# Kernel tuning notes

Measured on AMD Instinct MI355X. Metric: run time of the kernel, lower is better.

## Reference

```python
import jax, jax.numpy as jnp
import numpy as np

H = 128  # per-direction hidden size; bidirectional output = 256


def sru_layer(x, W, b):
    """One bidirectional SRU layer (use_selu=1).
    x: (L, B, n_in); W: (n_in, 2H*k); b: (4H,) = [f-bias(2H), r-bias(2H)].
    """
    L, B, n_in = x.shape
    k = W.shape[1] // (2 * H)  # 4 if n_in != 2H else 3
    U = (x @ W).reshape(L, B, 2, H, k)  # (L,B,dir,H,k)
    bf = b[: 2 * H].reshape(2, H)
    br = b[2 * H :].reshape(2, H)
    # highway input: learned projection (k==4) or the input itself split per direction
    xp = U[..., 3] if k == 4 else x.reshape(L, B, 2, H)
    # time-reverse the backward direction so a single scan serves both
    Us = jnp.stack([U[:, :, 0, :, :3], U[::-1, :, 1, :, :3]], axis=2)  # (L,B,2,H,3)
    xps = jnp.stack([xp[:, :, 0], xp[::-1, :, 1]], axis=2)  # (L,B,2,H)

    def step(c, t):
        u, xpt = t
        xt = u[..., 0]
        f = jax.nn.sigmoid(u[..., 1] + bf)
        r = jax.nn.sigmoid(u[..., 2] + br)
        c = f * c + (1.0 - f) * xt
        h = r * jax.nn.selu(c) + (1.0 - r) * xpt
        return c, h

    c0 = jnp.zeros((B, 2, H), x.dtype)
    _, hs = jax.lax.scan(step, c0, (Us, xps))  # hs: (L,B,2,H)
    # un-reverse backward direction, concat directions -> (L,B,2H)
    return jnp.concatenate([hs[:, :, 0], hs[::-1, :, 1]], axis=-1)


def setup_inputs() -> dict:
    key = jax.random.key(0)
    ks = jax.random.split(key, 6)
    L, B, D = 1024, 64, 128
    inp = {
        "input": jax.random.normal(ks[0], (L, B, D), jnp.float32),
        "W0": jax.random.normal(ks[1], (D, 4 * 2 * H), jnp.float32) / np.sqrt(D),
        "b0": jnp.zeros((4 * H,), jnp.float32),
        "gamma": jnp.ones((2 * H,), jnp.float32),
        "beta": jnp.zeros((2 * H,), jnp.float32),
    }
    for i, kk in zip((1, 2, 3), ks[2:5]):
        inp[f"W{i}"] = jax.random.normal(kk, (2 * H, 3 * 2 * H), jnp.float32) / np.sqrt(2 * H)
        inp[f"b{i}"] = jnp.zeros((4 * H,), jnp.float32)
    return inp


def reference(input, W0, b0, W1, b1, W2, b2, W3, b3, gamma, beta):
    x = sru_layer(input, W0, b0)
    x = sru_layer(x, W1, b1)
    x = sru_layer(x, W2, b2)
    x = sru_layer(x, W3, b3)  # (L,B,256)
    # permute(1,2,0) + avg_pool1d over full length + squeeze == mean over time
    feats = jnp.mean(x, axis=0)  # (B,256)
    mu = jnp.mean(feats, axis=-1, keepdims=True)
    var = jnp.mean(jnp.square(feats - mu), axis=-1, keepdims=True)
    return (feats - mu) / jnp.sqrt(var + 1e-5) * gamma + beta
```

## Files before the change

### kernel.cpp

```cpp
#include <hip/hip_runtime.h>
#include <math.h>

#define HID 128
#define LSEQ 1024
#define NB 64
#define SUB 32
#define NQG (LSEQ / SUB)
#define NCH 16384

typedef __attribute__((ext_vector_type(4))) float f32x4;
typedef __attribute__((ext_vector_type(8))) short bf16x8;
typedef __attribute__((ext_vector_type(8))) unsigned short u16x8;
typedef __attribute__((ext_vector_type(4))) unsigned short u16x4;

template <int N>
__device__ __forceinline__ void vmcntN() {
    asm volatile("s_waitcnt vmcnt(%0)" :: "n"(N) : "memory");
}

__device__ __forceinline__ unsigned short f2bf(float x) {
    union { float f; unsigned int u; } a; a.f = x;
    unsigned int r = a.u + 0x7FFFu + ((a.u >> 16) & 1u);
    return (unsigned short)(r >> 16);
}
__device__ __forceinline__ float bf2f(unsigned short h) {
    union { float f; unsigned int u; } a; a.u = ((unsigned int)h) << 16;
    return a.f;
}
__device__ __forceinline__ float sigmoidf_(float x) { return 1.0f / (1.0f + __expf(-x)); }
__device__ __forceinline__ float seluf_(float x) {
    const float sc = 1.0507009873554805f, al = 1.6732632423543772f;
    return x > 0.0f ? sc * x : sc * al * (__expf(x) - 1.0f);
}

__device__ __forceinline__ void gload16(const unsigned short* g, unsigned short* l) {
    __builtin_amdgcn_global_load_lds(
        (const __attribute__((address_space(1))) unsigned int*)g,
        (__attribute__((address_space(3))) unsigned int*)l, 16, 0, 0);
}

__global__ __launch_bounds__(256) void conv_wt(const float* __restrict__ W,
                                               unsigned short* __restrict__ Wt,
                                               int K, int N, int kw) {
    int idx = blockIdx.x * 256 + threadIdx.x;
    if (idx >= K * N) return;
    int k = idx / N, n = idx - k * N;
    const int dir = n / (128 * kw);
    const int rem = n - dir * 128 * kw;
    const int h = rem / kw, j = rem - h * kw;
    const int np = dir * 128 * kw + j * 128 + h;
    Wt[(size_t)np * K + k] = f2bf(W[idx]);
}

__global__ __launch_bounds__(256) void conv_in(const float* __restrict__ in,
                                               unsigned short* __restrict__ outp,
                                               int n4) {
    int idx = blockIdx.x * 256 + threadIdx.x;
    if (idx >= n4) return;
    const float4 v = *reinterpret_cast<const float4*>(in + (size_t)idx * 4);
    u16x4 w;
    w[0] = f2bf(v.x); w[1] = f2bf(v.y); w[2] = f2bf(v.z); w[3] = f2bf(v.w);
    *(u16x4*)(outp + (size_t)idx * 4) = w;
}

template <int K, int NC>
__global__ __launch_bounds__(256) void gemm_v5(const unsigned short* __restrict__ A,
                                               const unsigned short* __restrict__ Bt,
                                               unsigned short* __restrict__ C) {
    constexpr int NN = NC / 128;
    constexpr int NT = K / 64;
    constexpr int NSTEP = 4 * NT;
    __shared__ __align__(16) unsigned short smB[NT * 128 * 64];
    __shared__ __align__(16) unsigned short smA[4][4][2048];

    const int bid = blockIdx.x;
    const int mi = bid & 7;
    const int tt = bid >> 3;
    const int n = tt % NN;
    const int mg = (tt / NN) * 8 + mi;
    const int mb = mg * 512;
    const int n0 = n * 128;

    const int tid = threadIdx.x;
    const int w = tid >> 6, l = tid & 63;
    const int rlo = l & 15, g = l >> 4;
    const int kx = (l & 7) ^ (l >> 3);
    const int kswz = (rlo & 7) * 8;

#pragma unroll
    for (int kt = 0; kt < NT; ++kt)
#pragma unroll
        for (int rd = 0; rd < 4; ++rd) {
            const int col = rd * 32 + (tid >> 3);
            const int kxb = (tid & 7) ^ ((tid >> 3) & 7);
            gload16(Bt + (size_t)(n0 + col) * K + kt * 64 + kxb * 8,
                    &smB[kt * 8192 + rd * 2048 + tid * 8]);
        }

    auto stageA = [&](int s2) {
        const int mt2 = s2 / NT, kt2 = s2 % NT, sl = s2 & 3;
        const int rowb = mb + mt2 * 128 + w * 32;
#pragma unroll
        for (int i = 0; i < 4; ++i)
            gload16(A + (size_t)(rowb + i * 8 + (l >> 3)) * K + kt2 * 64 + kx * 8,
                    &smA[w][sl][i * 512 + l * 8]);
    };

    stageA(0); stageA(1); stageA(2);
    vmcntN<8>();
    __builtin_amdgcn_sched_barrier(0);
    __builtin_amdgcn_s_barrier();
    __builtin_amdgcn_sched_barrier(0);

    f32x4 acc[2][8];
#pragma unroll
    for (int s = 0; s < NSTEP; ++s) {
        const int mt = s / NT, kt = s % NT, slot = s & 3;
        if (kt == 0) {
#pragma unroll
            for (int mf = 0; mf < 2; ++mf)
#pragma unroll
                for (int nf = 0; nf < 8; ++nf) acc[mf][nf] = (f32x4){0.f, 0.f, 0.f, 0.f};
        }
        if (s + 3 < NSTEP) { stageA(s + 3); vmcntN<12>(); }
        else if (s + 3 == NSTEP) vmcntN<8>();
        else if (s + 2 == NSTEP) vmcntN<4>();
        else                     vmcntN<0>();
        __builtin_amdgcn_sched_barrier(0);

#pragma unroll
        for (int kk = 0; kk < 2; ++kk) {
            const int koff = (kk * 32 + g * 8) ^ kswz;
            bf16x8 af[2], bff[8];
#pragma unroll
            for (int mf = 0; mf < 2; ++mf)
                af[mf] = *(const bf16x8*)(&smA[w][slot][(mf * 16 + rlo) * 64 + koff]);
#pragma unroll
            for (int nf = 0; nf < 8; ++nf)
                bff[nf] = *(const bf16x8*)(&smB[kt * 8192 + (nf * 16 + rlo) * 64 + koff]);
#pragma unroll
            for (int mf = 0; mf < 2; ++mf)
#pragma unroll
                for (int nf = 0; nf < 8; ++nf)
                    acc[mf][nf] = __builtin_amdgcn_mfma_f32_16x16x32_bf16(
                        bff[nf], af[mf], acc[mf][nf], 0, 0, 0);
        }

        if (kt == NT - 1) {
            const int rowb = mb + mt * 128 + w * 32;
#pragma unroll
            for (int mf = 0; mf < 2; ++mf) {
                const size_t rbase = (size_t)(rowb + mf * 16 + rlo) * NC + n0 + g * 4;
#pragma unroll
                for (int nf = 0; nf < 8; ++nf) {
                    u16x4 v;
                    v[0] = f2bf(acc[mf][nf][0]); v[1] = f2bf(acc[mf][nf][1]);
                    v[2] = f2bf(acc[mf][nf][2]); v[3] = f2bf(acc[mf][nf][3]);
                    *(u16x4*)(&C[rbase + nf * 16]) = v;
                }
            }
        }
    }
}

template <int NC>
__global__ __launch_bounds__(256) void scanA(const unsigned short* __restrict__ U,
                                             const float* __restrict__ bias,
                                             float* __restrict__ aArr,
                                             float* __restrict__ bArr,
                                             int dirbase, int dbstride,
                                             int chmask, int chshift, int T) {
    const int gid = blockIdx.x * 256 + threadIdx.x;
    const int fc = gid & chmask;
    const int q = gid >> chshift;
    const int dir = dirbase + (fc >> 13);
    const int b = (fc >> 7) & 63, h = fc & 127;
    const int dbase = (fc >> 13) * dbstride;
    const float bfb = bias[dir * HID + h];

    float aa = 1.0f, cc = 0.0f;
#pragma unroll 4
    for (int i = 0; i < SUB; ++i) {
        const int s = q * SUB + i;
        const int t = dir ? (T - 1 - s) : s;
        const size_t m = (size_t)t * NB + b;
        const float u0 = bf2f(U[m * NC + dbase + h]);
        const float u1 = bf2f(U[m * NC + dbase + 128 + h]);
        const float f = sigmoidf_(u1 + bfb);
        cc = f * cc + (1.0f - f) * u0;
        aa *= f;
    }
    const int fcg = dir * 8192 + (fc & 8191);
    aArr[(size_t)q * NCH + fcg] = aa;
    bArr[(size_t)q * NCH + fcg] = cc;
}

template <int Q>
__global__ __launch_bounds__(256) void scanB(const float* __restrict__ aArr,
                                             const float* __restrict__ bArr,
                                             float* __restrict__ cin,
                                             float* __restrict__ carry,
                                             int init, int fcg0) {
    const int fcg = fcg0 + blockIdx.x * 256 + threadIdx.x;
    float a[Q], bb[Q];
#pragma unroll
    for (int q = 0; q < Q; ++q) {
        a[q]  = aArr[(size_t)q * NCH + fcg];
        bb[q] = bArr[(size_t)q * NCH + fcg];
    }
    float c = init ? 0.0f : carry[fcg];
#pragma unroll
    for (int q = 0; q < Q; ++q) {
        cin[(size_t)q * NCH + fcg] = c;
        c = a[q] * c + bb[q];
    }
    carry[fcg] = c;
}

template <int NC, bool XP_FROM_U, bool ACC>
__global__ __launch_bounds__(256) void scanC(const unsigned short* __restrict__ U,
                                             const unsigned short* __restrict__ Xprev,
                                             const float* __restrict__ bias,
                                             const float* __restrict__ cin,
                                             unsigned short* __restrict__ Xout,
                                             float* __restrict__ part,
                                             int dirbase, int dbstride,
                                             int chmask, int chshift,
                                             int T, int t0, int qg0) {
    const int gid = blockIdx.x * 256 + threadIdx.x;
    const int fc = gid & chmask;
    const int q = gid >> chshift;
    const int dir = dirbase + (fc >> 13);
    const int b = (fc >> 7) & 63, h = fc & 127;
    const int dbase = (fc >> 13) * dbstride;
    const float bfb = bias[dir * HID + h];
    const float brb = bias[2 * HID + dir * HID + h];
    const int fcg = dir * 8192 + (fc & 8191);

    float c = cin[(size_t)q * NCH + fcg];
    float psum = 0.0f;
#pragma unroll 4
    for (int i = 0; i < SUB; ++i) {
        const int s = q * SUB + i;
        const int t = dir ? (T - 1 - s) : s;
        const size_t m = (size_t)t * NB + b;
        const size_t xrow = ((size_t)(t0 + t) * NB + b) * (2 * HID) + dir * HID + h;
        const float u0 = bf2f(U[m * NC + dbase + h]);
        const float u1 = bf2f(U[m * NC + dbase + 128 + h]);
        const float u2 = bf2f(U[m * NC + dbase + 256 + h]);
        float xp;
        if constexpr (XP_FROM_U) xp = bf2f(U[m * NC + dbase + 384 + h]);
        else                     xp = bf2f(Xprev[xrow]);
        const float f = sigmoidf_(u1 + bfb);
        const float r = sigmoidf_(u2 + brb);
        c = f * c + (1.0f - f) * u0;
        const float ho = r * seluf_(c) + (1.0f - r) * xp;
        if constexpr (ACC) psum += ho;
        else               Xout[xrow] = f2bf(ho);
    }
    if constexpr (ACC)
        part[(size_t)(qg0 + q) * (NB * 256) + b * 256 + dir * HID + h] = psum;
}

__global__ __launch_bounds__(256) void pool2(const float* __restrict__ part,
                                             const float* __restrict__ gamma,
                                             const float* __restrict__ beta,
                                             float* __restrict__ out) {
    const int b = blockIdx.x, chn = threadIdx.x;
    float s = 0.0f;
#pragma unroll
    for (int i = 0; i < NQG; ++i) s += part[(size_t)i * (NB * 256) + b * 256 + chn];
    const float feat = s * (1.0f / LSEQ);
    __shared__ float red[256];
    red[chn] = feat; __syncthreads();
    for (int off = 128; off > 0; off >>= 1) { if (chn < off) red[chn] += red[chn + off]; __syncthreads(); }
    const float mu = red[0] * (1.0f / 256.0f);
    __syncthreads();
    const float d = feat - mu;
    red[chn] = d * d; __syncthreads();
    for (int off = 128; off > 0; off >>= 1) { if (chn < off) red[chn] += red[chn + off]; __syncthreads(); }
    const float var = red[0] * (1.0f / 256.0f);
    out[b * 256 + chn] = d * rsqrtf(var + 1e-5f) * gamma[chn] + beta[chn];
}

extern "C" void kernel_launch(void* const* d_in, const int* in_sizes, int n_in,
                              void* d_out, int out_size, void* d_ws, size_t ws_size,
                              hipStream_t stream) {
    const float* input = (const float*)d_in[0];
    const float* gamma = (const float*)d_in[3];
    const float* beta  = (const float*)d_in[4];
    const float* Wl[4] = { (const float*)d_in[1], (const float*)d_in[5],
                           (const float*)d_in[7], (const float*)d_in[9] };
    const float* bl[4] = { (const float*)d_in[2], (const float*)d_in[6],
                           (const float*)d_in[8], (const float*)d_in[10] };
    float* out = (float*)d_out;

    char* base = (char*)d_ws;
    size_t off = 0;
    auto alloc = [&](size_t bytes) { size_t o = off; off = (off + bytes + 255) & ~(size_t)255; return o; };

    unsigned short* Wt[4];
    Wt[0] = (unsigned short*)(base + alloc((size_t)1024 * 128 * 2));
    for (int i = 1; i < 4; ++i) Wt[i] = (unsigned short*)(base + alloc((size_t)768 * 256 * 2));
    unsigned short* Xa = (unsigned short*)(base + alloc((size_t)LSEQ * NB * 256 * 2));
    unsigned short* Xb = (unsigned short*)(base + alloc((size_t)LSEQ * NB * 256 * 2));
    unsigned short* Xc = (unsigned short*)(base + alloc((size_t)LSEQ * NB * 128 * 2));
    float* carry = (float*)(base + alloc((size_t)NCH * 4));
    float* aArr  = (float*)(base + alloc((size_t)32 * NCH * 4));
    float* bArr  = (float*)(base + alloc((size_t)32 * NCH * 4));
    float* cinArr= (float*)(base + alloc((size_t)32 * NCH * 4));
    float* part  = (float*)(base + alloc((size_t)NQG * NB * 256 * 4));
    if (ws_size < off + (1u << 21)) return;
    const size_t uavail = ws_size - off;
    unsigned short* U = (unsigned short*)(base + off);

    conv_in<<<(LSEQ * NB * 128 / 4 + 255) / 256, 256, 0, stream>>>(input, Xc, LSEQ * NB * 128 / 4);
    conv_wt<<<(128 * 1024 + 255) / 256, 256, 0, stream>>>(Wl[0], Wt[0], 128, 1024, 4);
    for (int i = 1; i < 4; ++i)
        conv_wt<<<(256 * 768 + 255) / 256, 256, 0, stream>>>(Wl[i], Wt[i], 256, 768, 3);

    const unsigned short* Xin[4] = { Xc, Xa, Xb, Xa };
    unsigned short* Xout[4] = { Xa, Xb, Xa, nullptr };

    if (uavail >= (size_t)LSEQ * NB * 1024 * 2) {
        const int T = LSEQ, Q = T / SUB;
        const dim3 sgrid(NCH * Q / 256);
        for (int layer = 0; layer < 4; ++layer) {
            const int kw = (layer == 0) ? 4 : 3;
            const int dbstride = 128 * kw;
            if (layer == 0)
                gemm_v5<128, 1024><<<dim3(8 * 128), 256, 0, stream>>>(Xin[0], Wt[0], U);
            else
                gemm_v5<256, 768><<<dim3(6 * 128), 256, 0, stream>>>(Xin[layer], Wt[layer], U);
            if (layer == 0)
                scanA<1024><<<sgrid, 256, 0, stream>>>(U, bl[0], aArr, bArr, 0, dbstride,
                                                       NCH - 1, 14, T);
            else
                scanA<768><<<sgrid, 256, 0, stream>>>(U, bl[layer], aArr, bArr, 0, dbstride,
                                                      NCH - 1, 14, T);
            scanB<32><<<NCH / 256, 256, 0, stream>>>(aArr, bArr, cinArr, carry, 1, 0);
            if (layer == 0)
                scanC<1024, true, false><<<sgrid, 256, 0, stream>>>(
                    U, nullptr, bl[0], cinArr, Xout[0], nullptr, 0, dbstride, NCH - 1, 14, T, 0, 0);
            else if (layer < 3)
                scanC<768, false, false><<<sgrid, 256, 0, stream>>>(
                    U, Xin[layer], bl[layer], cinArr, Xout[layer], nullptr, 0, dbstride,
                    NCH - 1, 14, T, 0, 0);
            else
                scanC<768, false, true><<<sgrid, 256, 0, stream>>>(
                    U, Xin[3], bl[3], cinArr, nullptr, part, 0, dbstride, NCH - 1, 14, T, 0, 0);
        }
    } else {
        int T = 0;
        for (int t = 512; t >= 64; t >>= 1)
            if ((size_t)t * NB * 512 * 2 <= uavail) { T = t; break; }
        if (T == 0) return;
        const int C = LSEQ / T, Q = T / SUB;
        const int nmg = T * NB / 512;
        const dim3 sgrid(8192 * Q / 256);
        for (int layer = 0; layer < 4; ++layer) {
            const int kw = (layer == 0) ? 4 : 3;
            const int K = (layer == 0) ? 128 : 256;
            const int Nc = 128 * kw;
            for (int dir = 0; dir < 2; ++dir) {
                const unsigned short* Bts = Wt[layer] + (size_t)dir * Nc * K;
                for (int cc = 0; cc < C; ++cc) {
                    const int ci = dir ? (C - 1 - cc) : cc;
                    const unsigned short* Ap = Xin[layer] + (size_t)ci * T * NB * K;
                    if (layer == 0)
                        gemm_v5<128, 512><<<dim3(4 * nmg), 256, 0, stream>>>(Ap, Bts, U);
                    else
                        gemm_v5<256, 384><<<dim3(3 * nmg), 256, 0, stream>>>(Ap, Bts, U);
                    if (layer == 0)
                        scanA<512><<<sgrid, 256, 0, stream>>>(U, bl[0], aArr, bArr, dir, 0,
                                                              8191, 13, T);
                    else
                        scanA<384><<<sgrid, 256, 0, stream>>>(U, bl[layer], aArr, bArr, dir, 0,
                                                              8191, 13, T);
                    if (Q == 16)
                        scanB<16><<<32, 256, 0, stream>>>(aArr, bArr, cinArr, carry,
                                                          cc == 0 ? 1 : 0, dir * 8192);
                    else
                        scanB<32><<<32, 256, 0, stream>>>(aArr, bArr, cinArr, carry,
                                                          cc == 0 ? 1 : 0, dir * 8192);
                    if (layer == 0)
                        scanC<512, true, false><<<sgrid, 256, 0, stream>>>(
                            U, nullptr, bl[0], cinArr, Xout[0], nullptr, dir, 0,
                            8191, 13, T, ci * T, ci * Q);
                    else if (layer < 3)
                        scanC<384, false, false><<<sgrid, 256, 0, stream>>>(
                            U, Xin[layer], bl[layer], cinArr, Xout[layer], nullptr, dir, 0,
                            8191, 13, T, ci * T, ci * Q);
                    else
                        scanC<384, false, true><<<sgrid, 256, 0, stream>>>(
                            U, Xin[3], bl[3], cinArr, nullptr, part, dir, 0,
                            8191, 13, T, ci * T, ci * Q);
                }
            }
        }
    }
    pool2<<<NB, 256, 0, stream>>>(part, gamma, beta, out);
}
```

Baseline: 404.3 us.

## Halve GEMM N-tile and load A fragments directly into registers

The GEMM kernel now uses a 64-wide N tile instead of 128, doubling the grid size, and drops the LDS staging of A. Each wave loads its A fragments straight from global memory into registers with a two-deep register double buffer, replacing the async global-to-LDS pipeline and its manual vmcnt waits. Less LDS per block and a launch bound of 3 are meant to raise occupancy and parallelism. In exchange, B tiles are reloaded by twice as many blocks, and A loads go through uncoalesced per-lane vector loads whose latency must be hidden by occupancy.

```diff
diff --git a/kernel.cpp b/kernel.cpp
--- a/kernel.cpp
+++ b/kernel.cpp
@@ -12,11 +12,6 @@
 typedef __attribute__((ext_vector_type(8))) short bf16x8;
 typedef __attribute__((ext_vector_type(8))) unsigned short u16x8;
 typedef __attribute__((ext_vector_type(4))) unsigned short u16x4;
-
-template <int N>
-__device__ __forceinline__ void vmcntN() {
-    asm volatile("s_waitcnt vmcnt(%0)" :: "n"(N) : "memory");
-}
 
 __device__ __forceinline__ unsigned short f2bf(float x) {
     union { float f; unsigned int u; } a; a.f = x;
@@ -64,14 +59,13 @@
 }
 
 template <int K, int NC>
-__global__ __launch_bounds__(256) void gemm_v5(const unsigned short* __restrict__ A,
-                                               const unsigned short* __restrict__ Bt,
-                                               unsigned short* __restrict__ C) {
-    constexpr int NN = NC / 128;
+__global__ __launch_bounds__(256, 3) void gemm_v6(const unsigned short* __restrict__ A,
+                                                  const unsigned short* __restrict__ Bt,
+                                                  unsigned short* __restrict__ C) {
+    constexpr int NN = NC / 64;
     constexpr int NT = K / 64;
     constexpr int NSTEP = 4 * NT;
-    __shared__ __align__(16) unsigned short smB[NT * 128 * 64];
-    __shared__ __align__(16) unsigned short smA[4][4][2048];
+    __shared__ __align__(16) unsigned short smB[NT * 4096];
 
     const int bid = blockIdx.x;
     const int mi = bid & 7;
@@ -79,80 +73,71 @@
     const int n = tt % NN;
     const int mg = (tt / NN) * 8 + mi;
     const int mb = mg * 512;
-    const int n0 = n * 128;
+    const int n0 = n * 64;
 
     const int tid = threadIdx.x;
     const int w = tid >> 6, l = tid & 63;
     const int rlo = l & 15, g = l >> 4;
-    const int kx = (l & 7) ^ (l >> 3);
     const int kswz = (rlo & 7) * 8;
 
 #pragma unroll
     for (int kt = 0; kt < NT; ++kt)
 #pragma unroll
-        for (int rd = 0; rd < 4; ++rd) {
+        for (int rd = 0; rd < 2; ++rd) {
             const int col = rd * 32 + (tid >> 3);
             const int kxb = (tid & 7) ^ ((tid >> 3) & 7);
             gload16(Bt + (size_t)(n0 + col) * K + kt * 64 + kxb * 8,
-                    &smB[kt * 8192 + rd * 2048 + tid * 8]);
-        }
-
-    auto stageA = [&](int s2) {
-        const int mt2 = s2 / NT, kt2 = s2 % NT, sl = s2 & 3;
-        const int rowb = mb + mt2 * 128 + w * 32;
-#pragma unroll
-        for (int i = 0; i < 4; ++i)
-            gload16(A + (size_t)(rowb + i * 8 + (l >> 3)) * K + kt2 * 64 + kx * 8,
-                    &smA[w][sl][i * 512 + l * 8]);
+                    &smB[kt * 4096 + rd * 2048 + tid * 8]);
+        }
+
+    const unsigned short* gA = A + ((size_t)mb + w * 32 + rlo) * K + g * 8;
+
+    bf16x8 af[2][2][2];
+    auto loadA = [&](int s, int buf) {
+        const int mt = s / NT, kt = s % NT;
+        const unsigned short* p = gA + (size_t)mt * 128 * K + kt * 64;
+#pragma unroll
+        for (int mf = 0; mf < 2; ++mf)
+#pragma unroll
+            for (int kk = 0; kk < 2; ++kk)
+                af[buf][mf][kk] = *(const bf16x8*)(p + (size_t)mf * 16 * K + kk * 32);
     };
 
-    stageA(0); stageA(1); stageA(2);
-    vmcntN<8>();
-    __builtin_amdgcn_sched_barrier(0);
-    __builtin_amdgcn_s_barrier();
-    __builtin_amdgcn_sched_barrier(0);
-
-    f32x4 acc[2][8];
+    loadA(0, 0);
+    __syncthreads();
+
+    f32x4 acc[2][4];
 #pragma unroll
     for (int s = 0; s < NSTEP; ++s) {
-        const int mt = s / NT, kt = s % NT, slot = s & 3;
+        const int mt = s / NT, kt = s % NT, cur = s & 1;
         if (kt == 0) {
 #pragma unroll
             for (int mf = 0; mf < 2; ++mf)
 #pragma unroll
-                for (int nf = 0; nf < 8; ++nf) acc[mf][nf] = (f32x4){0.f, 0.f, 0.f, 0.f};
-        }
-        if (s + 3 < NSTEP) { stageA(s + 3); vmcntN<12>(); }
-        else if (s + 3 == NSTEP) vmcntN<8>();
-        else if (s + 2 == NSTEP) vmcntN<4>();
-        else                     vmcntN<0>();
-        __builtin_amdgcn_sched_barrier(0);
-
+                for (int nf = 0; nf < 4; ++nf) acc[mf][nf] = (f32x4){0.f, 0.f, 0.f, 0.f};
+        }
+        if (s + 1 < NSTEP) loadA(s + 1, cur ^ 1);
 #pragma unroll
         for (int kk = 0; kk < 2; ++kk) {
             const int koff = (kk * 32 + g * 8) ^ kswz;
-            bf16x8 af[2], bff[8];
+            bf16x8 bff[4];
+#pragma unroll
+            for (int nf = 0; nf < 4; ++nf)
+                bff[nf] = *(const bf16x8*)(&smB[kt * 4096 + (nf * 16 + rlo) * 64 + koff]);
 #pragma unroll
             for (int mf = 0; mf < 2; ++mf)
-                af[mf] = *(const bf16x8*)(&smA[w][slot][(mf * 16 + rlo) * 64 + koff]);
-#pragma unroll
-            for (int nf = 0; nf < 8; ++nf)
-                bff[nf] = *(const bf16x8*)(&smB[kt * 8192 + (nf * 16 + rlo) * 64 + koff]);
-#pragma unroll
-            for (int mf = 0; mf < 2; ++mf)
-#pragma unroll
-                for (int nf = 0; nf < 8; ++nf)
+#pragma unroll
+                for (int nf = 0; nf < 4; ++nf)
                     acc[mf][nf] = __builtin_amdgcn_mfma_f32_16x16x32_bf16(
-                        bff[nf], af[mf], acc[mf][nf], 0, 0, 0);
-        }
-
+                        bff[nf], af[cur][mf][kk], acc[mf][nf], 0, 0, 0);
+        }
         if (kt == NT - 1) {
             const int rowb = mb + mt * 128 + w * 32;
 #pragma unroll
             for (int mf = 0; mf < 2; ++mf) {
                 const size_t rbase = (size_t)(rowb + mf * 16 + rlo) * NC + n0 + g * 4;
 #pragma unroll
-                for (int nf = 0; nf < 8; ++nf) {
+                for (int nf = 0; nf < 4; ++nf) {
                     u16x4 v;
                     v[0] = f2bf(acc[mf][nf][0]); v[1] = f2bf(acc[mf][nf][1]);
                     v[2] = f2bf(acc[mf][nf][2]); v[3] = f2bf(acc[mf][nf][3]);
@@ -329,9 +314,9 @@
             const int kw = (layer == 0) ? 4 : 3;
             const int dbstride = 128 * kw;
             if (layer == 0)
-                gemm_v5<128, 1024><<<dim3(8 * 128), 256, 0, stream>>>(Xin[0], Wt[0], U);
+                gemm_v6<128, 1024><<<dim3(16 * 128), 256, 0, stream>>>(Xin[0], Wt[0], U);
             else
-                gemm_v5<256, 768><<<dim3(6 * 128), 256, 0, stream>>>(Xin[layer], Wt[layer], U);
+                gemm_v6<256, 768><<<dim3(12 * 128), 256, 0, stream>>>(Xin[layer], Wt[layer], U);
             if (layer == 0)
                 scanA<1024><<<sgrid, 256, 0, stream>>>(U, bl[0], aArr, bArr, 0, dbstride,
                                                        NCH - 1, 14, T);
@@ -368,9 +353,9 @@
                     const int ci = dir ? (C - 1 - cc) : cc;
                     const unsigned short* Ap = Xin[layer] + (size_t)ci * T * NB * K;
                     if (layer == 0)
-                        gemm_v5<128, 512><<<dim3(4 * nmg), 256, 0, stream>>>(Ap, Bts, U);
+                        gemm_v6<128, 512><<<dim3(8 * nmg), 256, 0, stream>>>(Ap, Bts, U);
                     else
-                        gemm_v5<256, 384><<<dim3(3 * nmg), 256, 0, stream>>>(Ap, Bts, U);
+                        gemm_v6<256, 384><<<dim3(6 * nmg), 256, 0, stream>>>(Ap, Bts, U);
                     if (layer == 0)
                         scanA<512><<<sgrid, 256, 0, stream>>>(U, bl[0], aArr, bArr, dir, 0,
                                                               8191, 13, T);
```

After: 462.5 us. +14.4%, slower.
